# Kernel tuning notes

Measured on AMD Instinct MI355X. Metric: run time of the kernel, lower is better.

## Reference

```python
import jax, jax.numpy as jnp
import numpy as np

H = 12        # num_attention_heads
A = 16        # agent_num
C = 768       # hidden_size


def setup_inputs() -> dict:
    key = jax.random.key(0)
    ks = jax.random.split(key, 16)
    B, N = 8, 4096
    std = 0.02
    return {
        "s1_hidden_states": jax.random.normal(ks[0], (B, N, C), jnp.float32),
        "s2_hidden_states": jax.random.normal(ks[1], (B, N, C), jnp.float32),
        "Wq": jax.random.normal(ks[2], (C, C), jnp.float32) * std,
        "bq": jnp.zeros((C,), jnp.float32),
        "Wk": jax.random.normal(ks[3], (C, C), jnp.float32) * std,
        "bk": jnp.zeros((C,), jnp.float32),
        "Wv": jax.random.normal(ks[4], (C, C), jnp.float32) * std,
        "bv": jnp.zeros((C,), jnp.float32),
        "an_bias": jax.random.normal(ks[5], (H, A, 7, 7), jnp.float32) * std,
        "na_bias": jax.random.normal(ks[6], (H, A, 7, 7), jnp.float32) * std,
        "ah_bias": jax.random.normal(ks[7], (1, H, A, A, 1), jnp.float32) * std,
        "aw_bias": jax.random.normal(ks[8], (1, H, A, 1, A), jnp.float32) * std,
        "ha_bias": jax.random.normal(ks[9], (1, H, A, 1, A), jnp.float32) * std,
        "wa_bias": jax.random.normal(ks[10], (1, H, 1, A, A), jnp.float32) * std,
    }


def reference(s1_hidden_states, s2_hidden_states, Wq, bq, Wk, bk, Wv, bv,
              an_bias, na_bias, ah_bias, aw_bias, ha_bias, wa_bias):
    b, n, c = s1_hidden_states.shape
    m = s2_hidden_states.shape[1]
    hd = c // H
    scale = hd ** -0.5

    q = s1_hidden_states @ Wq.T + bq            # (b, n, c)
    k = s2_hidden_states @ Wk.T + bk            # (b, m, c)
    v = s2_hidden_states @ Wv.T + bv            # (b, m, c)

    # AdaptiveAvgPool1d(A) with n % A == 0 -> uniform chunk mean
    agent = q.reshape(b, A, n // A, c).mean(axis=2)  # (b, A, c)

    def heads(x):
        return x.reshape(b, -1, H, hd).transpose(0, 2, 1, 3)

    qh, kh, vh = heads(q), heads(k), heads(v)        # (b,H,·,hd)
    ah = heads(agent)                                # (b,H,A,hd)

    # stage 1: agent -> keys.  bias is constant per (h, a) row.
    pb1 = jax.image.resize(an_bias, (H, A, A, A), method='bilinear').reshape(1, H, A, A * A)
    pb2 = (ah_bias + aw_bias).reshape(1, H, A, A * A)
    pb = (pb1 + pb2).mean(axis=-1)                   # (1, H, A)
    agent_attn = jnp.einsum('bhad,bhmd->bham', ah * scale, kh) + pb[:, :, :, None]
    agent_attn = jax.nn.softmax(agent_attn, axis=-1)
    agent_v = jnp.einsum('bham,bhmd->bhad', agent_attn, vh)  # (b,H,A,hd)

    # stage 2: queries -> agents.
    ab1 = jax.image.resize(na_bias, (H, A, A, A), method='bilinear') \
            .reshape(1, H, A, A * A).transpose(0, 1, 3, 2)   # (1,H,A*A,A)
    ab2 = (ha_bias + wa_bias).reshape(1, H, A * A, A)
    ab = (ab1 + ab2).mean(axis=-2)                   # (1, H, A)
    q_attn = jnp.einsum('bhnd,bhad->bhna', qh * scale, ah) + ab[:, :, None, :]
    q_attn = jax.nn.softmax(q_attn, axis=-1)
    x = jnp.einsum('bhna,bhad->bhnd', q_attn, agent_v)  # (b,H,n,hd)
    return x.transpose(0, 2, 1, 3).reshape(b, n, c)
```

## Files before the change

### kernel.cpp

```cpp
#include <hip/hip_runtime.h>
#include <cstdint>
#include <cstddef>

typedef unsigned short ushort_t;
typedef unsigned int uint;

typedef __attribute__((ext_vector_type(8))) short short8;
typedef __attribute__((ext_vector_type(4))) float floatx4;

#define CDIM 768

__device__ __forceinline__ float bfu(ushort_t u) {
    return __uint_as_float(((uint)u) << 16);
}
__device__ __forceinline__ void bf2(uint u, float& lo, float& hi) {
    lo = __uint_as_float(u << 16);
    hi = __uint_as_float(u & 0xffff0000u);
}
__device__ __forceinline__ ushort_t f2bfu(float f) {
    uint u = __float_as_uint(f);
    u += 0x7fffu + ((u >> 16) & 1u);
    return (ushort_t)(u >> 16);
}
__device__ __forceinline__ uint pack2(float a, float b) {
    return (uint)f2bfu(a) | ((uint)f2bfu(b) << 16);
}
__device__ __forceinline__ uint cvt2(float lo, float hi) {
    uint r;
    asm("v_cvt_pk_bf16_f32 %0, %1, %2" : "=v"(r) : "v"(lo), "v"(hi));
    return r;
}
__device__ __forceinline__ short8 mk8(uint a, uint b, uint c, uint d) {
    union { uint4 u; short8 s; } x;
    x.u = (uint4){a, b, c, d};
    return x.s;
}
__device__ __forceinline__ void gload_lds16(const void* g, void* l) {
    __builtin_amdgcn_global_load_lds(
        (__attribute__((address_space(1))) void*)(uintptr_t)g,
        (__attribute__((address_space(3))) void*)l, 16, 0, 0);
}

__global__ __launch_bounds__(256) void cvt_all(
    const float* __restrict__ s1, const float* __restrict__ s2,
    const float* __restrict__ Wq, const float* __restrict__ Wk,
    const float* __restrict__ Wv, const float* __restrict__ bq,
    const float* __restrict__ na, const float* __restrict__ ha,
    const float* __restrict__ wa,
    ushort_t* __restrict__ abuf, ushort_t* __restrict__ wb,
    float* __restrict__ agent, float* __restrict__ ab)
{
    const int bid = blockIdx.x;
    if (bid < 24576) {
        const int m = (bid >= 12288);
        const int bx = bid - m * 12288;
        const float* src = (m == 0) ? s1 : s2;
        ushort_t* dst = abuf + (size_t)m * 25165824;
        const size_t i = ((size_t)bx * 256 + threadIdx.x) * 8;
        const float4 f0 = *(const float4*)(src + i);
        const float4 f1 = *(const float4*)(src + i + 4);
        uint4 u;
        u.x = pack2(f0.x, f0.y);
        u.y = pack2(f0.z, f0.w);
        u.z = pack2(f1.x, f1.y);
        u.w = pack2(f1.z, f1.w);
        *(uint4*)(dst + i) = u;
    } else if (bid < 25440) {
        const int wid = bid - 24576;
        const int m = wid / 288;
        const float* src = (m == 0) ? Wq : (m == 1 ? Wk : Wv);
        ushort_t* dst = wb + (size_t)m * 589824;
        const int i = ((wid % 288) * 256 + threadIdx.x) * 8;
        const float4 f0 = *(const float4*)(src + i);
        const float4 f1 = *(const float4*)(src + i + 4);
        uint4 u;
        u.x = pack2(f0.x, f0.y);
        u.y = pack2(f0.z, f0.w);
        u.z = pack2(f1.x, f1.y);
        u.w = pack2(f1.z, f1.w);
        *(uint4*)(dst + i) = u;
    } else if (bid < 25536) {
        const int bh = bid - 25440;
        const int h = bh % 12;
        for (int i = threadIdx.x; i < 1024; i += 256)
            agent[(size_t)bh * 1024 + i] = bq[h * 64 + (i & 63)];
    } else {
        const int t = threadIdx.x;
        if (t >= 192) return;
        const int h = t >> 4, a = t & 15;
        const float cw[7] = {2.25f, 2.34375f, 2.28125f, 2.25f, 2.28125f, 2.34375f, 2.25f};
        float acc = 0.f;
        const float* nb = na + (h * 16 + a) * 49;
        for (int i = 0; i < 7; ++i)
            for (int j = 0; j < 7; ++j)
                acc += cw[i] * cw[j] * nb[i * 7 + j];
        acc *= (1.0f / 256.0f);
        float s = 0.f;
        for (int p = 0; p < 16; ++p)
            s += ha[(h * 16 + p) * 16 + a] + wa[(h * 16 + p) * 16 + a];
        ab[t] = acc + s * (1.0f / 16.0f);
    }
}

__global__ __launch_bounds__(256, 2) void gemm_qkv(
    const ushort_t* __restrict__ ab, const ushort_t* __restrict__ wb,
    const float* __restrict__ bq, const float* __restrict__ bk, const float* __restrict__ bv,
    ushort_t* __restrict__ qo, ushort_t* __restrict__ ko, ushort_t* __restrict__ vo,
    float* __restrict__ agent)
{
    const int z = blockIdx.z;
    const ushort_t* A     = ab + (size_t)(z != 0) * 25165824;
    const ushort_t* W     = wb + (size_t)z * 589824;
    const float* bias     = (z == 0) ? bq : (z == 1 ? bk : bv);
    ushort_t* out         = (z == 0) ? qo : (z == 1 ? ko : vo);

    __shared__ ushort_t lds[17408];
    ushort_t* At = lds;
    ushort_t* Wt = lds + 8192;

    const int tid  = threadIdx.x;
    const int wave = tid >> 6;
    const int lane = tid & 63;
    const int wm = wave >> 1, wn = wave & 1;

    const int id   = blockIdx.x + (blockIdx.y << 8);
    const int id2  = (id & 7) * 192 + (id >> 3);
    const int row0 = (id2 / 6) * 128;
    const int col0 = (id2 % 6) * 128;

    const int sro = lane >> 3;
    const int sch = ((lane & 7) ^ sro) * 8;
    const ushort_t* gaBase = A + (size_t)(row0 + wave * 32 + sro) * CDIM + sch;
    const ushort_t* gwBase = W + (size_t)(col0 + wave * 32 + sro) * CDIM + sch;

    floatx4 acc[4][4];
    #pragma unroll
    for (int i = 0; i < 4; ++i)
        #pragma unroll
        for (int j = 0; j < 4; ++j)
            acc[i][j] = (floatx4){0.f, 0.f, 0.f, 0.f};

    const int q4 = lane >> 4, r16 = lane & 15;

    for (int kt = 0; kt < CDIM; kt += 64) {
        __syncthreads();
        #pragma unroll
        for (int i = 0; i < 4; ++i) {
            gload_lds16(gaBase + (size_t)i * 8 * CDIM + kt, &At[(wave * 32 + i * 8) * 64]);
            gload_lds16(gwBase + (size_t)i * 8 * CDIM + kt, &Wt[(wave * 32 + i * 8) * 64]);
        }
        __syncthreads();
        #pragma unroll
        for (int ks = 0; ks < 2; ++ks) {
            short8 af[4], bfr[4];
            #pragma unroll
            for (int mt = 0; mt < 4; ++mt) {
                const int row = wm * 64 + mt * 16 + r16;
                const int ch  = (ks * 4 + q4) ^ (row & 7);
                af[mt] = *(const short8*)&At[row * 64 + ch * 8];
            }
            #pragma unroll
            for (int nt = 0; nt < 4; ++nt) {
                const int row = wn * 64 + nt * 16 + r16;
                const int ch  = (ks * 4 + q4) ^ (row & 7);
                bfr[nt] = *(const short8*)&Wt[row * 64 + ch * 8];
            }
            #pragma unroll
            for (int mt = 0; mt < 4; ++mt)
                #pragma unroll
                for (int nt = 0; nt < 4; ++nt)
                    acc[mt][nt] = __builtin_amdgcn_mfma_f32_16x16x32_bf16(
                        af[mt], bfr[nt], acc[mt][nt], 0, 0, 0);
        }
    }

    __syncthreads();
    const int b = row0 >> 12;
    const int m_base = row0 & 4095;
    #pragma unroll
    for (int nt = 0; nt < 4; ++nt) {
        const int coll = wn * 64 + nt * 16 + r16;
        const float bb = bias[col0 + coll];
        float psum = 0.f;
        #pragma unroll
        for (int mt = 0; mt < 4; ++mt) {
            const int rowl = wm * 64 + mt * 16 + q4 * 4;
            #pragma unroll
            for (int r = 0; r < 4; ++r) {
                lds[(rowl + r) * 136 + coll] = f2bfu(acc[mt][nt][r] + bb);
                psum += acc[mt][nt][r];
            }
        }
        if (z == 0) {
            psum += __shfl_xor(psum, 16);
            psum += __shfl_xor(psum, 32);
            if (q4 == 0) {
                const int h = (col0 + coll) >> 6, d = (col0 + coll) & 63;
                atomicAdd(&agent[(size_t)(b * 12 + h) * 1024 + (m_base >> 8) * 64 + d],
                          psum * (1.0f / 256.0f));
            }
        }
    }
    __syncthreads();
    #pragma unroll
    for (int it = 0; it < 8; ++it) {
        const int task  = it * 256 + tid;
        const int chunk = task & 7;
        const int rh    = task >> 3;
        const int rowl  = rh >> 1, hl = rh & 1;
        const uint4 v = *(const uint4*)&lds[rowl * 136 + hl * 64 + chunk * 8];
        ushort_t* op = out + ((size_t)(b * 12 + (col0 >> 6) + hl) * 4096
                              + m_base + rowl) * 64 + chunk * 8;
        *(uint4*)op = v;
    }
}

__global__ __launch_bounds__(512) void stage1(
    const ushort_t* __restrict__ k_hm, const ushort_t* __restrict__ v_hm,
    const float* __restrict__ agent, float* __restrict__ Sp, float* __restrict__ avp)
{
    const int bh = blockIdx.x, z = blockIdx.y;
    const int tid = threadIdx.x;
    const int lane = tid & 63;
    const int w = tid >> 6;
    const int g = lane >> 4;
    const int t = lane & 15;
    __shared__ ushort_t E2[256 * 20];

    short8 ahA[2], ahE[2];
    #pragma unroll
    for (int k0 = 0; k0 < 2; ++k0) {
        const float* p = agent + (size_t)bh * 1024 + t * 64 + k0 * 32 + g * 8;
        const float4 f0 = *(const float4*)p;
        const float4 f1 = *(const float4*)(p + 4);
        const float v[8] = {f0.x, f0.y, f0.z, f0.w, f1.x, f1.y, f1.z, f1.w};
        uint u[4], e[4];
        #pragma unroll
        for (int j = 0; j < 4; ++j) {
            const float a0 = v[2*j] * 0.125f, a1 = v[2*j+1] * 0.125f;
            u[j] = cvt2(a0, a1);
            float b0, b1; bf2(u[j], b0, b1);
            e[j] = cvt2(a0 - b0, a1 - b1);
        }
        ahA[k0] = mk8(u[0], u[1], u[2], u[3]);
        ahE[k0] = mk8(e[0], e[1], e[2], e[3]);
    }

    const int m0 = z * 256;
    const ushort_t* kb = k_hm + ((size_t)bh * 4096 + m0) * 64;

    #pragma unroll
    for (int ti = 0; ti < 2; ++ti) {
        const int row = w * 32 + ti * 16 + t;
        const ushort_t* kp = kb + (size_t)row * 64 + g * 8;
        const short8 kB0 = *(const short8*)(kp);
        const short8 kB1 = *(const short8*)(kp + 32);
        floatx4 sc = {0.f, 0.f, 0.f, 0.f};
        sc = __builtin_amdgcn_mfma_f32_16x16x32_bf16(ahA[0], kB0, sc, 0, 0, 0);
        sc = __builtin_amdgcn_mfma_f32_16x16x32_bf16(ahA[1], kB1, sc, 0, 0, 0);
        sc = __builtin_amdgcn_mfma_f32_16x16x32_bf16(ahE[0], kB0, sc, 0, 0, 0);
        sc = __builtin_amdgcn_mfma_f32_16x16x32_bf16(ahE[1], kB1, sc, 0, 0, 0);
        const uint P0 = pack2(__expf(sc[0]), __expf(sc[1]));
        const uint P1 = pack2(__expf(sc[2]), __expf(sc[3]));
        *(uint2*)&E2[(size_t)row * 20 + g * 4] = make_uint2(P0, P1);
    }
    __syncthreads();

    const int gg = (tid >> 6) & 3;
    const int half = tid >> 8;
    const int ls = lane & 31;
    const int mseg = lane >> 5;
    const int d0 = ls * 2;
    const int mb = half * 128 + mseg * 64;
    const ushort_t* vb = v_hm + ((size_t)bh * 4096 + m0 + mb) * 64 + d0;
    float ac[4][2];
    float ss[4];
    #pragma unroll
    for (int a = 0; a < 4; ++a) { ac[a][0] = 0.f; ac[a][1] = 0.f; ss[a] = 0.f; }
    for (int ml = 0; ml < 64; ++ml) {
        const uint vv = *(const uint*)(vb + (size_t)ml * 64);
        float v0, v1;
        bf2(vv, v0, v1);
        const uint2 ee = *(const uint2*)&E2[(size_t)(mb + ml) * 20 + gg * 4];
        float e0, e1, e2, e3;
        bf2(ee.x, e0, e1);
        bf2(ee.y, e2, e3);
        ac[0][0] += e0 * v0; ac[0][1] += e0 * v1; ss[0] += e0;
        ac[1][0] += e1 * v0; ac[1][1] += e1 * v1; ss[1] += e1;
        ac[2][0] += e2 * v0; ac[2][1] += e2 * v1; ss[2] += e2;
        ac[3][0] += e3 * v0; ac[3][1] += e3 * v1; ss[3] += e3;
    }
    #pragma unroll
    for (int a = 0; a < 4; ++a) {
        ac[a][0] += __shfl_xor(ac[a][0], 32);
        ac[a][1] += __shfl_xor(ac[a][1], 32);
        ss[a]    += __shfl_xor(ss[a], 32);
    }
    const int z2 = z * 2 + half;
    if (mseg == 0) {
        float* avz = avp + (size_t)(z2 * 96 + bh) * 1024;
        #pragma unroll
        for (int a = 0; a < 4; ++a)
            *(float2*)&avz[(gg * 4 + a) * 64 + d0] = make_float2(ac[a][0], ac[a][1]);
        if (ls == 0) {
            #pragma unroll
            for (int a = 0; a < 4; ++a)
                Sp[((size_t)bh * 16 + gg * 4 + a) * 32 + z2] = ss[a];
        }
    }
}

__global__ __launch_bounds__(256) void redu(
    const float* __restrict__ avp, const float* __restrict__ Sp,
    float* __restrict__ avn_g)
{
    const int bh = blockIdx.x;
    const int tid = threadIdx.x;
    const int i4 = tid * 4;
    const int a = i4 >> 6;
    floatx4 num = {0.f, 0.f, 0.f, 0.f};
    #pragma unroll
    for (int zz = 0; zz < 32; ++zz)
        num += *(const floatx4*)&avp[(size_t)(zz * 96 + bh) * 1024 + i4];
    const float* sp = Sp + ((size_t)bh * 16 + a) * 32;
    floatx4 dv = {0.f, 0.f, 0.f, 0.f};
    #pragma unroll
    for (int j = 0; j < 8; ++j)
        dv += *(const floatx4*)(sp + j * 4);
    const float r = 1.0f / (dv[0] + dv[1] + dv[2] + dv[3]);
    *(floatx4*)&avn_g[(size_t)bh * 1024 + i4] = num * r;
}

__global__ __launch_bounds__(256) void stage2(
    const ushort_t* __restrict__ q_hm, const float* __restrict__ avn_g,
    const float* __restrict__ agent, const float* __restrict__ ab,
    float* __restrict__ out)
{
    const int nb = blockIdx.x;
    const int bh = blockIdx.y;
    const int b = bh / 12, h = bh % 12;
    const int tid = threadIdx.x;
    const int g = (tid >> 4) & 3;
    const int t = tid & 15;
    const int w = tid >> 6;
    __shared__ float avn[1024];

    {
        const int i4 = tid * 4;
        *(floatx4*)&avn[i4] = *(const floatx4*)&avn_g[(size_t)bh * 1024 + i4];
    }
    __syncthreads();

    short8 ahA[2], ahE[2];
    #pragma unroll
    for (int k0 = 0; k0 < 2; ++k0) {
        const float* p = agent + (size_t)bh * 1024 + t * 64 + k0 * 32 + g * 8;
        const float4 f0 = *(const float4*)p;
        const float4 f1 = *(const float4*)(p + 4);
        const float v[8] = {f0.x, f0.y, f0.z, f0.w, f1.x, f1.y, f1.z, f1.w};
        uint u[4], e[4];
        #pragma unroll
        for (int j = 0; j < 4; ++j) {
            const float a0 = v[2*j] * 0.125f, a1 = v[2*j+1] * 0.125f;
            u[j] = cvt2(a0, a1);
            float b0, b1; bf2(u[j], b0, b1);
            e[j] = cvt2(a0 - b0, a1 - b1);
        }
        ahA[k0] = mk8(u[0], u[1], u[2], u[3]);
        ahE[k0] = mk8(e[0], e[1], e[2], e[3]);
    }

    short8 avf[4], ave[4];
    #pragma unroll
    for (int dt = 0; dt < 4; ++dt) {
        uint u[4] = {0, 0, 0, 0}, e[4] = {0, 0, 0, 0};
        if (g < 2) {
            #pragma unroll
            for (int j = 0; j < 4; ++j) {
                const float a0 = avn[(8*g + 2*j)     * 64 + dt * 16 + t];
                const float a1 = avn[(8*g + 2*j + 1) * 64 + dt * 16 + t];
                u[j] = cvt2(a0, a1);
                float b0, b1; bf2(u[j], b0, b1);
                e[j] = cvt2(a0 - b0, a1 - b1);
            }
        }
        avf[dt] = mk8(u[0], u[1], u[2], u[3]);
        ave[dt] = mk8(e[0], e[1], e[2], e[3]);
    }

    float abv[4];
    #pragma unroll
    for (int r = 0; r < 4; ++r) abv[r] = ab[h * 16 + 4 * g + r];

    const int src0 = (t + 32 * g) & 63;
    const int src1 = (src0 + 16) & 63;
    const int n0 = nb * 256 + w * 64;
    const ushort_t* qb = q_hm + ((size_t)bh * 4096 + n0) * 64;
    float* ob = out + ((size_t)b * 4096 + n0) * CDIM + h * 64;

    #pragma unroll
    for (int ti = 0; ti < 4; ++ti) {
        const ushort_t* qp = qb + (size_t)(ti * 16 + t) * 64 + g * 8;
        const short8 qB0 = *(const short8*)(qp);
        const short8 qB1 = *(const short8*)(qp + 32);

        floatx4 sc = {0.f, 0.f, 0.f, 0.f};
        sc = __builtin_amdgcn_mfma_f32_16x16x32_bf16(ahA[0], qB0, sc, 0, 0, 0);
        sc = __builtin_amdgcn_mfma_f32_16x16x32_bf16(ahA[1], qB1, sc, 0, 0, 0);
        sc = __builtin_amdgcn_mfma_f32_16x16x32_bf16(ahE[0], qB0, sc, 0, 0, 0);
        sc = __builtin_amdgcn_mfma_f32_16x16x32_bf16(ahE[1], qB1, sc, 0, 0, 0);

        const float e0 = __expf(sc[0] + abv[0]);
        const float e1 = __expf(sc[1] + abv[1]);
        const float e2 = __expf(sc[2] + abv[2]);
        const float e3 = __expf(sc[3] + abv[3]);
        float s = e0 + e1 + e2 + e3;
        s += __shfl_xor(s, 16);
        s += __shfl_xor(s, 32);
        const float rs = 1.0f / s;
        const float p0 = e0 * rs, p1 = e1 * rs, p2 = e2 * rs, p3 = e3 * rs;

        const uint P0 = cvt2(p0, p1), P1 = cvt2(p2, p3);
        float q0, q1, q2, q3;
        bf2(P0, q0, q1); bf2(P1, q2, q3);
        const uint E0 = cvt2(p0 - q0, p1 - q1), E1 = cvt2(p2 - q2, p3 - q3);

        uint w0 = __shfl(P0, src0), w1 = __shfl(P1, src0);
        uint w2 = __shfl(P0, src1), w3 = __shfl(P1, src1);
        uint x0 = __shfl(E0, src0), x1 = __shfl(E1, src0);
        uint x2 = __shfl(E0, src1), x3 = __shfl(E1, src1);
        if (g >= 2) { w0 = w1 = w2 = w3 = 0; x0 = x1 = x2 = x3 = 0; }
        const short8 pf = mk8(w0, w1, w2, w3);
        const short8 pe = mk8(x0, x1, x2, x3);

        float* op = ob + (size_t)(ti * 16 + t) * CDIM + 4 * g;
        #pragma unroll
        for (int dt = 0; dt < 4; ++dt) {
            floatx4 od = {0.f, 0.f, 0.f, 0.f};
            od = __builtin_amdgcn_mfma_f32_16x16x32_bf16(avf[dt], pf, od, 0, 0, 0);
            od = __builtin_amdgcn_mfma_f32_16x16x32_bf16(avf[dt], pe, od, 0, 0, 0);
            od = __builtin_amdgcn_mfma_f32_16x16x32_bf16(ave[dt], pf, od, 0, 0, 0);
            *(floatx4*)(op + dt * 16) = od;
        }
    }
}

extern "C" void kernel_launch(void* const* d_in, const int* in_sizes, int n_in,
                              void* d_out, int out_size, void* d_ws, size_t ws_size,
                              hipStream_t stream) {
    (void)in_sizes; (void)n_in; (void)out_size; (void)ws_size;
    const float* s1 = (const float*)d_in[0];
    const float* s2 = (const float*)d_in[1];
    const float* Wq = (const float*)d_in[2];
    const float* bq = (const float*)d_in[3];
    const float* Wk = (const float*)d_in[4];
    const float* bk = (const float*)d_in[5];
    const float* Wv = (const float*)d_in[6];
    const float* bv = (const float*)d_in[7];
    const float* na = (const float*)d_in[9];
    const float* ha = (const float*)d_in[12];
    const float* wa = (const float*)d_in[13];
    float* out = (float*)d_out;

    char* ws = (char*)d_ws;
    ushort_t* q_hm = (ushort_t*)(ws);
    ushort_t* k_hm = (ushort_t*)(ws + 50331648);
    ushort_t* v_hm = (ushort_t*)(ws + 100663296);
    float* agent   = (float*)(ws + 150994944);
    float* Sp      = (float*)(ws + 151388160);
    float* ab      = (float*)(ws + 151584768);
    float* avn_g   = (float*)(ws + 151585536);
    ushort_t* wb   = (ushort_t*)(ws + 151978752);
    ushort_t* abuf = (ushort_t*)(ws + 155517696);
    float* avp     = (float*)(ws + 155517696);

    cvt_all  <<<dim3(25537),     256, 0, stream>>>(s1, s2, Wq, Wk, Wv, bq,
                                                   na, ha, wa, abuf, wb, agent, ab);
    gemm_qkv <<<dim3(256, 6, 3), 256, 0, stream>>>(abuf, wb, bq, bk, bv,
                                                   q_hm, k_hm, v_hm, agent);
    stage1   <<<dim3(96, 16),    512, 0, stream>>>(k_hm, v_hm, agent, Sp, avp);
    redu     <<<dim3(96),        256, 0, stream>>>(avp, Sp, avn_g);
    stage2   <<<dim3(16, 96),    256, 0, stream>>>(q_hm, avn_g, agent, ab, out);
}
```

Baseline: 263.0 us.

## Rewrite QKV GEMM as 256x256 tile with double-buffered 8-wave pipelined schedule

The QKV projection GEMM now uses 512-thread blocks computing 256x256 output tiles instead of 128x128, with a double-buffered LDS layout. Global-to-LDS loads for the next k-slice are interleaved with MFMA quadrants under explicit barriers, waitcnts and setprio, so memory latency is hidden behind compute rather than fully serialised. The epilogue writes the tile out in two halves through LDS. It uses 128KB of LDS and many accumulator registers, so only one block fits per CU, and the fixed grid of 384 tiles per projection may leave tail imbalance.

Measured after the change: 266.1 us. About the same (+1.2%).

```diff
diff --git a/kernel.cpp b/kernel.cpp
--- a/kernel.cpp
+++ b/kernel.cpp
@@ -102,7 +102,7 @@
     }
 }
 
-__global__ __launch_bounds__(256, 2) void gemm_qkv(
+__global__ __launch_bounds__(512, 1) void gemm_qkv(
     const ushort_t* __restrict__ ab, const ushort_t* __restrict__ wb,
     const float* __restrict__ bq, const float* __restrict__ bk, const float* __restrict__ bv,
     ushort_t* __restrict__ qo, ushort_t* __restrict__ ko, ushort_t* __restrict__ vo,
@@ -114,104 +114,195 @@
     const float* bias     = (z == 0) ? bq : (z == 1 ? bk : bv);
     ushort_t* out         = (z == 0) ? qo : (z == 1 ? ko : vo);
 
-    __shared__ ushort_t lds[17408];
-    ushort_t* At = lds;
-    ushort_t* Wt = lds + 8192;
+    __shared__ ushort_t lds[65536];
 
     const int tid  = threadIdx.x;
     const int wave = tid >> 6;
     const int lane = tid & 63;
-    const int wm = wave >> 1, wn = wave & 1;
-
-    const int id   = blockIdx.x + (blockIdx.y << 8);
-    const int id2  = (id & 7) * 192 + (id >> 3);
-    const int row0 = (id2 / 6) * 128;
-    const int col0 = (id2 % 6) * 128;
+    const int wm = wave >> 2, wn = wave & 3;
+
+    const int id  = blockIdx.x;
+    const int id2 = (id & 7) * 48 + (id >> 3);
+    const int row0 = (id2 / 3) * 256;
+    const int col0 = (id2 % 3) * 256;
 
     const int sro = lane >> 3;
     const int sch = ((lane & 7) ^ sro) * 8;
-    const ushort_t* gaBase = A + (size_t)(row0 + wave * 32 + sro) * CDIM + sch;
-    const ushort_t* gwBase = W + (size_t)(col0 + wave * 32 + sro) * CDIM + sch;
-
-    floatx4 acc[4][4];
-    #pragma unroll
-    for (int i = 0; i < 4; ++i)
+    const ushort_t* gaBase = A + (size_t)(row0 + wave * 8 + sro) * CDIM + sch;
+    const ushort_t* gwBase = W + (size_t)(col0 + wave * 8 + sro) * CDIM + sch;
+
+    auto stageA = [&](int half, int t) {
+        const ushort_t* g = gaBase + (size_t)(half * 128) * CDIM + t * 64;
+        ushort_t* l = &lds[(t & 1) * 16384 + (half * 128 + wave * 8) * 64];
+        gload_lds16(g, l);
+        gload_lds16(g + (size_t)64 * CDIM, l + 64 * 64);
+    };
+    auto stageB = [&](int half, int t) {
+        const ushort_t* g = gwBase + (size_t)(half * 128) * CDIM + t * 64;
+        ushort_t* l = &lds[32768 + (t & 1) * 16384 + (half * 128 + wave * 8) * 64];
+        gload_lds16(g, l);
+        gload_lds16(g + (size_t)64 * CDIM, l + 64 * 64);
+    };
+
+    floatx4 acc[8][4];
+    #pragma unroll
+    for (int i = 0; i < 8; ++i)
         #pragma unroll
         for (int j = 0; j < 4; ++j)
             acc[i][j] = (floatx4){0.f, 0.f, 0.f, 0.f};
 
     const int q4 = lane >> 4, r16 = lane & 15;
 
-    for (int kt = 0; kt < CDIM; kt += 64) {
-        __syncthreads();
-        #pragma unroll
-        for (int i = 0; i < 4; ++i) {
-            gload_lds16(gaBase + (size_t)i * 8 * CDIM + kt, &At[(wave * 32 + i * 8) * 64]);
-            gload_lds16(gwBase + (size_t)i * 8 * CDIM + kt, &Wt[(wave * 32 + i * 8) * 64]);
-        }
-        __syncthreads();
-        #pragma unroll
-        for (int ks = 0; ks < 2; ++ks) {
-            short8 af[4], bfr[4];
-            #pragma unroll
-            for (int mt = 0; mt < 4; ++mt) {
-                const int row = wm * 64 + mt * 16 + r16;
-                const int ch  = (ks * 4 + q4) ^ (row & 7);
-                af[mt] = *(const short8*)&At[row * 64 + ch * 8];
-            }
-            #pragma unroll
-            for (int nt = 0; nt < 4; ++nt) {
-                const int row = wn * 64 + nt * 16 + r16;
-                const int ch  = (ks * 4 + q4) ^ (row & 7);
-                bfr[nt] = *(const short8*)&Wt[row * 64 + ch * 8];
-            }
-            #pragma unroll
-            for (int mt = 0; mt < 4; ++mt)
-                #pragma unroll
-                for (int nt = 0; nt < 4; ++nt)
-                    acc[mt][nt] = __builtin_amdgcn_mfma_f32_16x16x32_bf16(
-                        af[mt], bfr[nt], acc[mt][nt], 0, 0, 0);
-        }
-    }
-
-    __syncthreads();
+    short8 af[4][2], bf0[2][2], bf1[2][2];
+
+    #define RD_A(MH, BUF)                                                        \
+        _Pragma("unroll")                                                        \
+        for (int mtl = 0; mtl < 4; ++mtl) {                                      \
+            const int row = wm * 128 + (MH) * 64 + mtl * 16 + r16;               \
+            _Pragma("unroll")                                                    \
+            for (int ks = 0; ks < 2; ++ks) {                                     \
+                const int ch = (ks * 4 + q4) ^ (row & 7);                        \
+                af[mtl][ks] = *(const short8*)&lds[(BUF) * 16384 + row * 64 + ch * 8]; \
+            }                                                                    \
+        }
+    #define RD_B(DST, NH, BUF)                                                   \
+        _Pragma("unroll")                                                        \
+        for (int ntl = 0; ntl < 2; ++ntl) {                                      \
+            const int row = wn * 64 + (NH) * 32 + ntl * 16 + r16;                \
+            _Pragma("unroll")                                                    \
+            for (int ks = 0; ks < 2; ++ks) {                                     \
+                const int ch = (ks * 4 + q4) ^ (row & 7);                        \
+                DST[ntl][ks] = *(const short8*)&lds[32768 + (BUF) * 16384 + row * 64 + ch * 8]; \
+            }                                                                    \
+        }
+    #define MFMA_Q(MH, NH, BF)                                                   \
+        _Pragma("unroll")                                                        \
+        for (int mtl = 0; mtl < 4; ++mtl)                                        \
+            _Pragma("unroll")                                                    \
+            for (int ntl = 0; ntl < 2; ++ntl)                                    \
+                _Pragma("unroll")                                                \
+                for (int ks = 0; ks < 2; ++ks)                                   \
+                    acc[(MH)*4+mtl][(NH)*2+ntl] =                                \
+                        __builtin_amdgcn_mfma_f32_16x16x32_bf16(                 \
+                            af[mtl][ks], BF[ntl][ks], acc[(MH)*4+mtl][(NH)*2+ntl], 0, 0, 0);
+    #define SYNC_MFMA(MH, NH, BF)                                                \
+        __builtin_amdgcn_s_barrier();                                            \
+        asm volatile("s_waitcnt lgkmcnt(0)" ::: "memory");                       \
+        __builtin_amdgcn_sched_barrier(0);                                       \
+        __builtin_amdgcn_s_setprio(1);                                           \
+        MFMA_Q(MH, NH, BF);                                                      \
+        __builtin_amdgcn_s_setprio(0);
+
+    stageB(0, 0); stageB(1, 0); stageA(0, 0); stageA(1, 0);
+    stageB(0, 1); stageB(1, 1);
+    asm volatile("s_waitcnt vmcnt(4)" ::: "memory");
+    __builtin_amdgcn_s_barrier();
+
+    #pragma unroll 1
+    for (int it = 0; it < 6; ++it) {
+        const bool full = (it < 5);
+        RD_B(bf0, 0, 0); RD_A(0, 0);
+        stageA(0, 2 * it + 1);
+        SYNC_MFMA(0, 0, bf0);
+        __builtin_amdgcn_s_barrier();
+
+        RD_B(bf1, 1, 0);
+        stageA(1, 2 * it + 1);
+        SYNC_MFMA(0, 1, bf1);
+        __builtin_amdgcn_s_barrier();
+
+        RD_A(1, 0);
+        if (full) stageB(0, 2 * it + 2);
+        SYNC_MFMA(1, 1, bf1);
+        __builtin_amdgcn_s_barrier();
+
+        if (full) stageB(1, 2 * it + 2);
+        SYNC_MFMA(1, 0, bf0);
+        if (full) { asm volatile("s_waitcnt vmcnt(4)" ::: "memory"); }
+        else      { asm volatile("s_waitcnt vmcnt(0)" ::: "memory"); }
+        __builtin_amdgcn_s_barrier();
+
+        RD_B(bf0, 0, 1); RD_A(0, 1);
+        if (full) stageA(0, 2 * it + 2);
+        SYNC_MFMA(0, 0, bf0);
+        __builtin_amdgcn_s_barrier();
+
+        RD_B(bf1, 1, 1);
+        if (full) stageA(1, 2 * it + 2);
+        SYNC_MFMA(0, 1, bf1);
+        __builtin_amdgcn_s_barrier();
+
+        RD_A(1, 1);
+        if (full) stageB(0, 2 * it + 3);
+        SYNC_MFMA(1, 1, bf1);
+        __builtin_amdgcn_s_barrier();
+
+        if (full) stageB(1, 2 * it + 3);
+        SYNC_MFMA(1, 0, bf0);
+        if (full) { asm volatile("s_waitcnt vmcnt(4)" ::: "memory"); }
+        __builtin_amdgcn_s_barrier();
+    }
+    #undef RD_A
+    #undef RD_B
+    #undef MFMA_Q
+    #undef SYNC_MFMA
+
     const int b = row0 >> 12;
     const int m_base = row0 & 4095;
-    #pragma unroll
-    for (int nt = 0; nt < 4; ++nt) {
-        const int coll = wn * 64 + nt * 16 + r16;
-        const float bb = bias[col0 + coll];
-        float psum = 0.f;
-        #pragma unroll
-        for (int mt = 0; mt < 4; ++mt) {
-            const int rowl = wm * 64 + mt * 16 + q4 * 4;
+
+    if (z == 0) {
+        #pragma unroll
+        for (int nt = 0; nt < 4; ++nt) {
+            const int coll = wn * 64 + nt * 16 + r16;
+            float psum = 0.f;
             #pragma unroll
-            for (int r = 0; r < 4; ++r) {
-                lds[(rowl + r) * 136 + coll] = f2bfu(acc[mt][nt][r] + bb);
-                psum += acc[mt][nt][r];
-            }
-        }
-        if (z == 0) {
+            for (int mt = 0; mt < 8; ++mt)
+                #pragma unroll
+                for (int r = 0; r < 4; ++r)
+                    psum += acc[mt][nt][r];
             psum += __shfl_xor(psum, 16);
             psum += __shfl_xor(psum, 32);
             if (q4 == 0) {
-                const int h = (col0 + coll) >> 6, d = (col0 + coll) & 63;
+                const int col = col0 + coll;
+                const int h = col >> 6, d = col & 63;
                 atomicAdd(&agent[(size_t)(b * 12 + h) * 1024 + (m_base >> 8) * 64 + d],
                           psum * (1.0f / 256.0f));
             }
         }
     }
-    __syncthreads();
-    #pragma unroll
-    for (int it = 0; it < 8; ++it) {
-        const int task  = it * 256 + tid;
-        const int chunk = task & 7;
-        const int rh    = task >> 3;
-        const int rowl  = rh >> 1, hl = rh & 1;
-        const uint4 v = *(const uint4*)&lds[rowl * 136 + hl * 64 + chunk * 8];
-        ushort_t* op = out + ((size_t)(b * 12 + (col0 >> 6) + hl) * 4096
-                              + m_base + rowl) * 64 + chunk * 8;
-        *(uint4*)op = v;
+
+    #pragma unroll 1
+    for (int hc = 0; hc < 2; ++hc) {
+        __builtin_amdgcn_s_barrier();
+        if (wm == hc) {
+            #pragma unroll
+            for (int nt = 0; nt < 4; ++nt) {
+                const int coll = wn * 64 + nt * 16 + r16;
+                const float bb = bias[col0 + coll];
+                #pragma unroll
+                for (int mh = 0; mh < 2; ++mh)
+                    #pragma unroll
+                    for (int mtl = 0; mtl < 4; ++mtl) {
+                        const int rowl = mh * 64 + mtl * 16 + q4 * 4;
+                        #pragma unroll
+                        for (int r = 0; r < 4; ++r)
+                            lds[(rowl + r) * 264 + coll] =
+                                f2bfu(acc[mh * 4 + mtl][nt][r] + bb);
+                    }
+            }
+        }
+        __builtin_amdgcn_s_barrier();
+        #pragma unroll
+        for (int itr = 0; itr < 8; ++itr) {
+            const int task  = itr * 512 + tid;
+            const int chunk = task & 7;
+            const int rh    = task >> 3;
+            const int rowl  = rh >> 2, hl = rh & 3;
+            const uint4 v = *(const uint4*)&lds[rowl * 264 + hl * 64 + chunk * 8];
+            ushort_t* op = out + ((size_t)(b * 12 + (col0 >> 6) + hl) * 4096
+                                  + m_base + hc * 128 + rowl) * 64 + chunk * 8;
+            *(uint4*)op = v;
+        }
     }
 }
 
@@ -476,7 +567,7 @@
 
     cvt_all  <<<dim3(25537),     256, 0, stream>>>(s1, s2, Wq, Wk, Wv, bq,
                                                    na, ha, wa, abuf, wb, agent, ab);
-    gemm_qkv <<<dim3(256, 6, 3), 256, 0, stream>>>(abuf, wb, bq, bk, bv,
+    gemm_qkv <<<dim3(384, 1, 3), 512, 0, stream>>>(abuf, wb, bq, bk, bv,
                                                    q_hm, k_hm, v_hm, agent);
     stage1   <<<dim3(96, 16),    512, 0, stream>>>(k_hm, v_hm, agent, Sp, avp);
     redu     <<<dim3(96),        256, 0, stream>>>(avp, Sp, avn_g);
```
